# Performance work log

Hardware: AMD Instinct MI355X
Metric: run time of the kernel (lower is better)

Reference implementation:

```python
import jax, jax.numpy as jnp
import numpy as np

H = 1024          # hidden_size
I = 2048          # intermediate_size (per routed expert; shared uses I*num_shared)
E = 8             # num_routed_experts
B, S = 2, 1024


def setup_inputs() -> dict:
    key = jax.random.key(0)
    ks = jax.random.split(key, 8)
    sc_h = 1.0 / np.sqrt(H)
    sc_i = 1.0 / np.sqrt(I)
    return {
        "hidden_states": jax.random.normal(ks[0], (B, S, H), jnp.float32),
        "gate_w": jax.random.normal(ks[1], (H, E), jnp.float32) * sc_h,      # router
        "sh_gate": jax.random.normal(ks[2], (H, I), jnp.float32) * sc_h,     # shared SwiGLU
        "sh_up": jax.random.normal(ks[3], (H, I), jnp.float32) * sc_h,
        "sh_down": jax.random.normal(ks[4], (I, H), jnp.float32) * sc_i,
        "rt_gate": jax.random.normal(ks[5], (E, H, I), jnp.float32) * sc_h,  # stacked routed experts
        "rt_up": jax.random.normal(ks[6], (E, H, I), jnp.float32) * sc_h,
        "rt_down": jax.random.normal(ks[7], (E, I, H), jnp.float32) * sc_i,
    }


def _swiglu(x, wg, wu, wd):
    return (jax.nn.silu(x @ wg) * (x @ wu)) @ wd


def reference(hidden_states, gate_w, sh_gate, sh_up, sh_down, rt_gate, rt_up, rt_down):
    b, s, h = hidden_states.shape
    x = hidden_states.reshape(-1, h)                      # [T, H]
    logits = x @ gate_w                                   # [T, E]
    # top-1 routing: score = sigmoid(max logit), expert = argmax
    top_val = jnp.max(logits, axis=-1, keepdims=True)     # [T, 1]
    top_id = jnp.argmax(logits, axis=-1)                  # [T]
    score = jax.nn.sigmoid(top_val)
    xs = x * score                                        # scale tokens BEFORE expert (Llama4)
    # exact dense-masked equivalent of sort/dispatch/per-expert SwiGLU/scatter-combine:
    # every expert is applied to all tokens, then the one-hot mask selects the
    # assigned expert's output per token (identical math to ragged dispatch).
    g = jnp.einsum('th,ehi->eti', xs, rt_gate)            # [E, T, I]
    u = jnp.einsum('th,ehi->eti', xs, rt_up)
    act = jax.nn.silu(g) * u
    y = jnp.einsum('eti,eih->eth', act, rt_down)          # [E, T, H]
    onehot = jax.nn.one_hot(top_id, E, dtype=x.dtype)     # [T, E]
    routed = jnp.einsum('eth,te->th', y, onehot)          # [T, H]
    shared = _swiglu(x, sh_gate, sh_up, sh_down)          # [T, H]
    return (shared + routed).reshape(b, s, h)
```

## Files before the change

### kernel.cpp

```cpp
#include <hip/hip_runtime.h>
#include <cstdint>
#include <cstddef>

#define T_TOK 2048
#define HDIM  1024
#define IDIM  2048
#define NEXP  8

#define BM 128
#define BK1 32
#define BK2 64
#define BN2 64
#define MAXPAD 3072
#define SH_TILES 16
#define RT_TILES 24

typedef __attribute__((ext_vector_type(8))) short short8;
typedef __attribute__((ext_vector_type(4))) short short4v;
typedef __attribute__((ext_vector_type(4))) float float4v;

__device__ __forceinline__ short f2bf(float f) {
  uint32_t u = __float_as_uint(f);
  u += 0x7fffu + ((u >> 16) & 1u);
  return (short)(u >> 16);
}

__device__ __forceinline__ void gload_lds16(const void* g, void* l) {
  __builtin_amdgcn_global_load_lds(
      (const __attribute__((address_space(1))) uint32_t*)g,
      (__attribute__((address_space(3))) uint32_t*)l, 16, 0, 0);
}

__device__ __forceinline__ int swz(int c) { return c ^ ((c >> 4) & 3); }
__device__ __forceinline__ int swz64(int c) { return c ^ ((c >> 3) & 7); }


__global__ __launch_bounds__(256) void zero_init(int* __restrict__ counts,
                                                 int* __restrict__ perm) {
  int i = threadIdx.x;
  if (i < NEXP) counts[i] = 0;
  for (int p = i; p < MAXPAD; p += 256) perm[p] = 0;
}

__global__ __launch_bounds__(256) void router_kernel(
    const float* __restrict__ x, const float* __restrict__ gw,
    short* __restrict__ xbf, short* __restrict__ xsbf,
    int* __restrict__ expert_id, int* __restrict__ slot,
    int* __restrict__ counts) {
  int wv = threadIdx.x >> 6, lane = threadIdx.x & 63;
  int t = blockIdx.x * 4 + wv;
  const float* xr = x + (size_t)t * HDIM;
  float4v xv[4];
  float lg[NEXP];
#pragma unroll
  for (int e = 0; e < NEXP; e++) lg[e] = 0.f;
#pragma unroll
  for (int p = 0; p < 4; p++) {
    xv[p] = *(const float4v*)(xr + p * 256 + lane * 4);
#pragma unroll
    for (int c = 0; c < 4; c++) {
      int h = p * 256 + lane * 4 + c;
      float4v g0 = *(const float4v*)(gw + (size_t)h * NEXP);
      float4v g1 = *(const float4v*)(gw + (size_t)h * NEXP + 4);
      float xc = xv[p][c];
      lg[0] += xc * g0[0]; lg[1] += xc * g0[1];
      lg[2] += xc * g0[2]; lg[3] += xc * g0[3];
      lg[4] += xc * g1[0]; lg[5] += xc * g1[1];
      lg[6] += xc * g1[2]; lg[7] += xc * g1[3];
    }
  }
#pragma unroll
  for (int ofs = 1; ofs < 64; ofs <<= 1) {
#pragma unroll
    for (int e = 0; e < NEXP; e++) lg[e] += __shfl_xor(lg[e], ofs, 64);
  }
  int be = 0;
  float bv = lg[0];
#pragma unroll
  for (int e = 1; e < NEXP; e++) {
    if (lg[e] > bv) { bv = lg[e]; be = e; }
  }
  float score = 1.f / (1.f + __expf(-bv));
  if (lane == 0) {
    expert_id[t] = be;
    slot[t] = atomicAdd(&counts[be], 1);
  }
#pragma unroll
  for (int p = 0; p < 4; p++) {
    short4v b, bs;
#pragma unroll
    for (int c = 0; c < 4; c++) {
      b[c] = f2bf(xv[p][c]);
      bs[c] = f2bf(xv[p][c] * score);
    }
    *(short4v*)(xbf + (size_t)t * HDIM + p * 256 + lane * 4) = b;
    *(short4v*)(xsbf + (size_t)t * HDIM + p * 256 + lane * 4) = bs;
  }
}

__global__ void prefix_kernel(const int* __restrict__ counts, int* __restrict__ pad_off) {
  if (threadIdx.x == 0 && blockIdx.x == 0) {
    int run = 0;
    for (int e = 0; e < NEXP; e++) {
      pad_off[e] = run;
      run += (counts[e] + BM - 1) & ~(BM - 1);
    }
    pad_off[NEXP] = run;
  }
}

__global__ __launch_bounds__(256) void build_perm(
    const int* __restrict__ expert_id, const int* __restrict__ slot,
    const int* __restrict__ pad_off, int* __restrict__ perm) {
  int t = blockIdx.x * 256 + threadIdx.x;
  int e = expert_id[t];
  perm[pad_off[e] + slot[t]] = t;
}


__global__ __launch_bounds__(256) void transpose_all(
    const float* __restrict__ shg, const float* __restrict__ shu,
    const float* __restrict__ rtg, const float* __restrict__ rtu,
    short* __restrict__ shg_t, short* __restrict__ shu_t,
    short* __restrict__ rtg_t, short* __restrict__ rtu_t,
    const float* __restrict__ shd, const float* __restrict__ rtd,
    short* __restrict__ shd_t, short* __restrict__ rtd_t) {
  __shared__ __align__(16) short t[64][66];
  int zz = blockIdx.z;
  int tid = threadIdx.x;
  int tr = tid >> 4, tc = (tid & 15) * 4;
  int oc = tid >> 2, rs = (tid & 3) * 16;
  if (zz < 9) {
    const float *s0, *s1;
    short *d0, *d1;
    if (zz == 0) { s0 = shg; s1 = shu; d0 = shg_t; d1 = shu_t; }
    else {
      size_t o = (size_t)(zz - 1) * HDIM * IDIM;
      s0 = rtg + o; s1 = rtu + o; d0 = rtg_t + o; d1 = rtu_t + o;
    }
    const int R = HDIM, C = IDIM;
    int r0 = blockIdx.y * 64, c0 = blockIdx.x * 64;
#pragma unroll
    for (int pass = 0; pass < 2; pass++) {
      const float* s = pass ? s1 : s0;
      short* d = pass ? d1 : d0;
      if (pass) __syncthreads();
#pragma unroll
      for (int i = 0; i < 4; i++) {
        float4v v = *(const float4v*)(s + (size_t)(r0 + tr + i * 16) * C + c0 + tc);
        int w0 = (int)(unsigned short)f2bf(v[0]) | ((int)f2bf(v[1]) << 16);
        int w1 = (int)(unsigned short)f2bf(v[2]) | ((int)f2bf(v[3]) << 16);
        int* p = (int*)&t[tr + i * 16][tc];
        p[0] = w0;
        p[1] = w1;
      }
      __syncthreads();
      short8 o0, o1;
#pragma unroll
      for (int j = 0; j < 8; j++) { o0[j] = t[rs + j][oc]; o1[j] = t[rs + 8 + j][oc]; }
      short* dp = d + (size_t)(c0 + oc) * R + r0 + rs;
      *(short8*)dp = o0;
      *(short8*)(dp + 8) = o1;
    }
  } else {
    int z = zz - 9;
    const float* s = (z == 0) ? shd : rtd + (size_t)(z - 1) * IDIM * HDIM;
    short* d = (z == 0) ? shd_t : rtd_t + (size_t)(z - 1) * IDIM * HDIM;
    const int R = IDIM, C = HDIM;
    int r0 = blockIdx.x * 64, c0 = blockIdx.y * 64;
#pragma unroll
    for (int i = 0; i < 4; i++) {
      float4v v = *(const float4v*)(s + (size_t)(r0 + tr + i * 16) * C + c0 + tc);
      int w0 = (int)(unsigned short)f2bf(v[0]) | ((int)f2bf(v[1]) << 16);
      int w1 = (int)(unsigned short)f2bf(v[2]) | ((int)f2bf(v[3]) << 16);
      int* p = (int*)&t[tr + i * 16][tc];
      p[0] = w0;
      p[1] = w1;
    }
    __syncthreads();
    short8 o0, o1;
#pragma unroll
    for (int j = 0; j < 8; j++) { o0[j] = t[rs + j][oc]; o1[j] = t[rs + 8 + j][oc]; }
    short* dp = d + (size_t)(c0 + oc) * R + r0 + rs;
    *(short8*)dp = o0;
    *(short8*)(dp + 8) = o1;
  }
}


__global__ __launch_bounds__(256) void gemm1_swiglu(
    const short* __restrict__ xbf, const short* __restrict__ xsbf,
    const short* __restrict__ shg_t, const short* __restrict__ shu_t,
    const short* __restrict__ rtg_t, const short* __restrict__ rtu_t,
    short* __restrict__ act_sh, short* __restrict__ act_rt,
    const int* __restrict__ pad_off, const int* __restrict__ perm) {
  __shared__ __align__(1024) short sA[2][BM * BK1];
  __shared__ __align__(1024) short sBg[2][BM * BK1];
  __shared__ __align__(1024) short sBu[2][BM * BK1];
  int tid = threadIdx.x, lane = tid & 63, wv = tid >> 6;
  int C0 = blockIdx.x * 128;
  int y = blockIdx.y;
  const short *A, *Bg, *Bu;
  short* act;
  int R0;
  bool routed = (y >= SH_TILES);
  if (!routed) {
    A = xbf; Bg = shg_t; Bu = shu_t; act = act_sh; R0 = y * BM;
  } else {
    R0 = (y - SH_TILES) * BM;
    if (R0 >= pad_off[NEXP]) return;
    int e = 0;
    while (pad_off[e + 1] <= R0) e++;
    size_t o = (size_t)e * HDIM * IDIM;
    A = xsbf; Bg = rtg_t + o; Bu = rtu_t + o; act = act_rt;
  }
  int c0 = swz(tid), c1 = swz(tid + 256);
  int r0c = c0 >> 2, r1c = c1 >> 2;
  int ar0 = routed ? perm[R0 + r0c] : R0 + r0c;
  int ar1 = routed ? perm[R0 + r1c] : R0 + r1c;
  size_t gA0 = (size_t)ar0 * HDIM + (c0 & 3) * 8;
  size_t gA1 = (size_t)ar1 * HDIM + (c1 & 3) * 8;
  size_t gB0 = (size_t)(C0 + r0c) * HDIM + (c0 & 3) * 8;
  size_t gB1 = (size_t)(C0 + r1c) * HDIM + (c1 & 3) * 8;

  float4v accg[4][4], accu[4][4];
  float4v z4 = {0.f, 0.f, 0.f, 0.f};
#pragma unroll
  for (int i = 0; i < 4; i++)
#pragma unroll
    for (int j = 0; j < 4; j++) { accg[i][j] = z4; accu[i][j] = z4; }

  const int wrow = (wv >> 1) * 64, wcol = (wv & 1) * 64;
  const int mrow = lane & 15, h4 = lane >> 4;
  int aoff[4], boff[4];
#pragma unroll
  for (int i = 0; i < 4; i++)
    aoff[i] = swz(((wrow + i * 16 + mrow) << 2) + h4) * 8;
#pragma unroll
  for (int j = 0; j < 4; j++)
    boff[j] = swz(((wcol + j * 16 + mrow) << 2) + h4) * 8;

  gload_lds16(A + gA0, sA[0] + tid * 8);
  gload_lds16(A + gA1, sA[0] + (tid + 256) * 8);
  gload_lds16(Bg + gB0, sBg[0] + tid * 8);
  gload_lds16(Bg + gB1, sBg[0] + (tid + 256) * 8);
  gload_lds16(Bu + gB0, sBu[0] + tid * 8);
  gload_lds16(Bu + gB1, sBu[0] + (tid + 256) * 8);

  int cur = 0;
  for (int k0 = 0; k0 < HDIM; k0 += BK1) {
    __syncthreads();
    int kn = k0 + BK1;
    if (kn < HDIM) {
      short* nA = sA[cur ^ 1];
      short* nG = sBg[cur ^ 1];
      short* nU = sBu[cur ^ 1];
      gload_lds16(A + gA0 + kn, nA + tid * 8);
      gload_lds16(A + gA1 + kn, nA + (tid + 256) * 8);
      gload_lds16(Bg + gB0 + kn, nG + tid * 8);
      gload_lds16(Bg + gB1 + kn, nG + (tid + 256) * 8);
      gload_lds16(Bu + gB0 + kn, nU + tid * 8);
      gload_lds16(Bu + gB1 + kn, nU + (tid + 256) * 8);
    }
    const short* cA = sA[cur];
    const short* cG = sBg[cur];
    const short* cU = sBu[cur];
    short8 af[4], bg[4], bu[4];
#pragma unroll
    for (int i = 0; i < 4; i++) af[i] = *(const short8*)(cA + aoff[i]);
#pragma unroll
    for (int j = 0; j < 4; j++) {
      bg[j] = *(const short8*)(cG + boff[j]);
      bu[j] = *(const short8*)(cU + boff[j]);
    }
#pragma unroll
    for (int i = 0; i < 4; i++)
#pragma unroll
      for (int j = 0; j < 4; j++) {
        accg[i][j] = __builtin_amdgcn_mfma_f32_16x16x32_bf16(af[i], bg[j], accg[i][j], 0, 0, 0);
        accu[i][j] = __builtin_amdgcn_mfma_f32_16x16x32_bf16(af[i], bu[j], accu[i][j], 0, 0, 0);
      }
    cur ^= 1;
  }
  int qrow = h4 * 4, col = mrow;
#pragma unroll
  for (int i = 0; i < 4; i++)
#pragma unroll
    for (int j = 0; j < 4; j++)
#pragma unroll
      for (int r = 0; r < 4; r++) {
        int row = R0 + wrow + i * 16 + qrow + r;
        int c = C0 + wcol + j * 16 + col;
        float g = accg[i][j][r], u = accu[i][j][r];
        float sv = g / (1.f + __expf(-g)) * u;
        act[(size_t)row * IDIM + c] = f2bf(sv);
      }
}


__global__ __launch_bounds__(256) void gemm2_down(
    const short* __restrict__ act_sh, const short* __restrict__ act_rt,
    const short* __restrict__ shd_t, const short* __restrict__ rtd_t,
    float* __restrict__ out, float* __restrict__ rt_out,
    const int* __restrict__ pad_off, const int* __restrict__ counts,
    const int* __restrict__ perm) {
  __shared__ __align__(1024) short sA[2][BM * BK2];
  __shared__ __align__(1024) short sB[2][BN2 * BK2];
  int tid = threadIdx.x, lane = tid & 63, wv = tid >> 6;
  int C0 = blockIdx.x * BN2;
  int y = blockIdx.y;
  const short *A, *Bd;
  int R0, e = 0;
  bool routed = (y >= SH_TILES);
  if (!routed) {
    A = act_sh; Bd = shd_t; R0 = y * BM;
  } else {
    R0 = (y - SH_TILES) * BM;
    if (R0 >= pad_off[NEXP]) return;
    while (pad_off[e + 1] <= R0) e++;
    A = act_rt; Bd = rtd_t + (size_t)e * IDIM * HDIM;
  }
  size_t gA[4], gB[2];
#pragma unroll
  for (int q = 0; q < 4; q++) {
    int c = swz64(tid + 256 * q);
    gA[q] = (size_t)(R0 + (c >> 3)) * IDIM + (c & 7) * 8;
  }
#pragma unroll
  for (int q = 0; q < 2; q++) {
    int c = swz64(tid + 256 * q);
    gB[q] = (size_t)(C0 + (c >> 3)) * IDIM + (c & 7) * 8;
  }

  float4v acc[2][4];
  float4v z4 = {0.f, 0.f, 0.f, 0.f};
#pragma unroll
  for (int i = 0; i < 2; i++)
#pragma unroll
    for (int j = 0; j < 4; j++) acc[i][j] = z4;

  const int wrow = wv * 32;
  const int mrow = lane & 15, h4 = lane >> 4;
  int aoff[2][2], boff[4][2];
#pragma unroll
  for (int i = 0; i < 2; i++)
#pragma unroll
    for (int ks = 0; ks < 2; ks++)
      aoff[i][ks] = swz64(((wrow + i * 16 + mrow) << 3) + ks * 4 + h4) * 8;
#pragma unroll
  for (int j = 0; j < 4; j++)
#pragma unroll
    for (int ks = 0; ks < 2; ks++)
      boff[j][ks] = swz64(((j * 16 + mrow) << 3) + ks * 4 + h4) * 8;

#pragma unroll
  for (int q = 0; q < 4; q++) gload_lds16(A + gA[q], sA[0] + (tid + 256 * q) * 8);
#pragma unroll
  for (int q = 0; q < 2; q++) gload_lds16(Bd + gB[q], sB[0] + (tid + 256 * q) * 8);

  int cur = 0;
  for (int k0 = 0; k0 < IDIM; k0 += BK2) {
    __syncthreads();
    int kn = k0 + BK2;
    if (kn < IDIM) {
      short* nA = sA[cur ^ 1];
      short* nB = sB[cur ^ 1];
#pragma unroll
      for (int q = 0; q < 4; q++) gload_lds16(A + gA[q] + kn, nA + (tid + 256 * q) * 8);
#pragma unroll
      for (int q = 0; q < 2; q++) gload_lds16(Bd + gB[q] + kn, nB + (tid + 256 * q) * 8);
    }
    const short* cA = sA[cur];
    const short* cB = sB[cur];
#pragma unroll
    for (int ks = 0; ks < 2; ks++) {
      short8 af[2], bf4[4];
#pragma unroll
      for (int i = 0; i < 2; i++) af[i] = *(const short8*)(cA + aoff[i][ks]);
#pragma unroll
      for (int j = 0; j < 4; j++) bf4[j] = *(const short8*)(cB + boff[j][ks]);
#pragma unroll
      for (int i = 0; i < 2; i++)
#pragma unroll
        for (int j = 0; j < 4; j++)
          acc[i][j] = __builtin_amdgcn_mfma_f32_16x16x32_bf16(af[i], bf4[j], acc[i][j], 0, 0, 0);
    }
    cur ^= 1;
  }
  int qrow = h4 * 4, col = mrow;
#pragma unroll
  for (int i = 0; i < 2; i++)
#pragma unroll
    for (int j = 0; j < 4; j++)
#pragma unroll
      for (int r = 0; r < 4; r++) {
        int row = R0 + wrow + i * 16 + qrow + r;
        int c = C0 + j * 16 + col;
        float v = acc[i][j][r];
        if (!routed) {
          out[(size_t)row * HDIM + c] = v;
        } else if (row - pad_off[e] < counts[e]) {
          rt_out[(size_t)perm[row] * HDIM + c] = v;
        }
      }
}

__global__ __launch_bounds__(256) void add_routed(float* __restrict__ out,
                                                  const float* __restrict__ rt_out) {
  size_t i = ((size_t)blockIdx.x * 256 + threadIdx.x) * 4;
  float4v a = *(const float4v*)(out + i);
  float4v b = *(const float4v*)(rt_out + i);
  a[0] += b[0]; a[1] += b[1]; a[2] += b[2]; a[3] += b[3];
  *(float4v*)(out + i) = a;
}


extern "C" void kernel_launch(void* const* d_in, const int* in_sizes, int n_in,
                              void* d_out, int out_size, void* d_ws, size_t ws_size,
                              hipStream_t stream) {
  const float* x       = (const float*)d_in[0];
  const float* gate_w  = (const float*)d_in[1];
  const float* sh_gate = (const float*)d_in[2];
  const float* sh_up   = (const float*)d_in[3];
  const float* sh_down = (const float*)d_in[4];
  const float* rt_gate = (const float*)d_in[5];
  const float* rt_up   = (const float*)d_in[6];
  const float* rt_down = (const float*)d_in[7];
  float* out = (float*)d_out;

  char* w = (char*)d_ws;
  const size_t MB = 1024 * 1024;
  short* xbf    = (short*)(w + 0 * MB);
  short* xsbf   = (short*)(w + 4 * MB);
  short* act_sh = (short*)(w + 8 * MB);
  short* act_rt = (short*)(w + 16 * MB);
  float* rt_out = (float*)(w + 28 * MB);
  short* shg_t  = (short*)(w + 36 * MB);
  short* shu_t  = (short*)(w + 40 * MB);
  short* shd_t  = (short*)(w + 44 * MB);
  short* rtg_t  = (short*)(w + 48 * MB);
  short* rtu_t  = (short*)(w + 80 * MB);
  short* rtd_t  = (short*)(w + 112 * MB);
  int* ints     = (int*)(w + 144 * MB);
  int* counts    = ints;
  int* pad_off   = ints + 8;
  int* expert_id = ints + 32;
  int* slot      = ints + 32 + 2048;
  int* perm      = ints + 32 + 4096;

  zero_init<<<1, 256, 0, stream>>>(counts, perm);
  router_kernel<<<T_TOK / 4, 256, 0, stream>>>(x, gate_w, xbf, xsbf, expert_id, slot, counts);
  prefix_kernel<<<1, 64, 0, stream>>>(counts, pad_off);
  build_perm<<<T_TOK / 256, 256, 0, stream>>>(expert_id, slot, pad_off, perm);

  transpose_all<<<dim3(32, 16, 18), 256, 0, stream>>>(
      sh_gate, sh_up, rt_gate, rt_up, shg_t, shu_t, rtg_t, rtu_t,
      sh_down, rt_down, shd_t, rtd_t);

  gemm1_swiglu<<<dim3(IDIM / 128, SH_TILES + RT_TILES), 256, 0, stream>>>(
      xbf, xsbf, shg_t, shu_t, rtg_t, rtu_t, act_sh, act_rt, pad_off, perm);

  gemm2_down<<<dim3(HDIM / BN2, SH_TILES + RT_TILES), 256, 0, stream>>>(
      act_sh, act_rt, shd_t, rtd_t, out, rt_out, pad_off, counts, perm);

  add_routed<<<(T_TOK * HDIM) / (256 * 4), 256, 0, stream>>>(out, rt_out);
}
```

Before: 424.1 us.

## Triple-buffer both GEMMs with explicit vmcnt waits and 512-thread gemm1

Both GEMM kernels move from double-buffered LDS staging with __syncthreads to a three-stage ring. Explicit s_waitcnt vmcnt and raw s_barrier let two tiles of loads stay in flight while MFMAs run, and s_setprio raises wave priority around the MFMA block. gemm1 now uses 512 threads with 8 waves, each computing a 64x32 subtile, and gemm2's K step drops from 64 to 32 to fit the extra buffer. This is meant to hide global-load latency and raise occupancy, at the cost of more barriers per unit of K work and halved per-wave reuse in gemm1.

```diff
diff --git a/kernel.cpp b/kernel.cpp
--- a/kernel.cpp
+++ b/kernel.cpp
@@ -9,7 +9,7 @@
 
 #define BM 128
 #define BK1 32
-#define BK2 64
+#define BK2 32
 #define BN2 64
 #define MAXPAD 3072
 #define SH_TILES 16
@@ -32,7 +32,6 @@
 }
 
 __device__ __forceinline__ int swz(int c) { return c ^ ((c >> 4) & 3); }
-__device__ __forceinline__ int swz64(int c) { return c ^ ((c >> 3) & 7); }
 
 
 __global__ __launch_bounds__(256) void zero_init(int* __restrict__ counts,
@@ -188,15 +187,20 @@
 }
 
 
-__global__ __launch_bounds__(256) void gemm1_swiglu(
+#define G1_STAGE(b, kk) do { \
+    gload_lds16(A + gA + (kk), sA[b] + tid * 8);   \
+    gload_lds16(Bg + gB + (kk), sBg[b] + tid * 8); \
+    gload_lds16(Bu + gB + (kk), sBu[b] + tid * 8); } while (0)
+
+__global__ __launch_bounds__(512, 2) void gemm1_swiglu(
     const short* __restrict__ xbf, const short* __restrict__ xsbf,
     const short* __restrict__ shg_t, const short* __restrict__ shu_t,
     const short* __restrict__ rtg_t, const short* __restrict__ rtu_t,
     short* __restrict__ act_sh, short* __restrict__ act_rt,
     const int* __restrict__ pad_off, const int* __restrict__ perm) {
-  __shared__ __align__(1024) short sA[2][BM * BK1];
-  __shared__ __align__(1024) short sBg[2][BM * BK1];
-  __shared__ __align__(1024) short sBu[2][BM * BK1];
+  __shared__ __align__(1024) short sA[3][BM * BK1];
+  __shared__ __align__(1024) short sBg[3][BM * BK1];
+  __shared__ __align__(1024) short sBu[3][BM * BK1];
   int tid = threadIdx.x, lane = tid & 63, wv = tid >> 6;
   int C0 = blockIdx.x * 128;
   int y = blockIdx.y;
@@ -214,79 +218,72 @@
     size_t o = (size_t)e * HDIM * IDIM;
     A = xsbf; Bg = rtg_t + o; Bu = rtu_t + o; act = act_rt;
   }
-  int c0 = swz(tid), c1 = swz(tid + 256);
-  int r0c = c0 >> 2, r1c = c1 >> 2;
+  int c0 = swz(tid);
+  int r0c = c0 >> 2;
   int ar0 = routed ? perm[R0 + r0c] : R0 + r0c;
-  int ar1 = routed ? perm[R0 + r1c] : R0 + r1c;
-  size_t gA0 = (size_t)ar0 * HDIM + (c0 & 3) * 8;
-  size_t gA1 = (size_t)ar1 * HDIM + (c1 & 3) * 8;
-  size_t gB0 = (size_t)(C0 + r0c) * HDIM + (c0 & 3) * 8;
-  size_t gB1 = (size_t)(C0 + r1c) * HDIM + (c1 & 3) * 8;
-
-  float4v accg[4][4], accu[4][4];
+  size_t gA = (size_t)ar0 * HDIM + (c0 & 3) * 8;
+  size_t gB = (size_t)(C0 + r0c) * HDIM + (c0 & 3) * 8;
+
+  float4v accg[4][2], accu[4][2];
   float4v z4 = {0.f, 0.f, 0.f, 0.f};
 #pragma unroll
   for (int i = 0; i < 4; i++)
 #pragma unroll
-    for (int j = 0; j < 4; j++) { accg[i][j] = z4; accu[i][j] = z4; }
-
-  const int wrow = (wv >> 1) * 64, wcol = (wv & 1) * 64;
+    for (int j = 0; j < 2; j++) { accg[i][j] = z4; accu[i][j] = z4; }
+
+  const int wrow = (wv >> 2) * 64, wcol = (wv & 3) * 32;
   const int mrow = lane & 15, h4 = lane >> 4;
-  int aoff[4], boff[4];
+  int aoff[4], boff[2];
 #pragma unroll
   for (int i = 0; i < 4; i++)
     aoff[i] = swz(((wrow + i * 16 + mrow) << 2) + h4) * 8;
 #pragma unroll
-  for (int j = 0; j < 4; j++)
+  for (int j = 0; j < 2; j++)
     boff[j] = swz(((wcol + j * 16 + mrow) << 2) + h4) * 8;
 
-  gload_lds16(A + gA0, sA[0] + tid * 8);
-  gload_lds16(A + gA1, sA[0] + (tid + 256) * 8);
-  gload_lds16(Bg + gB0, sBg[0] + tid * 8);
-  gload_lds16(Bg + gB1, sBg[0] + (tid + 256) * 8);
-  gload_lds16(Bu + gB0, sBu[0] + tid * 8);
-  gload_lds16(Bu + gB1, sBu[0] + (tid + 256) * 8);
+  G1_STAGE(0, 0);
+  G1_STAGE(1, BK1);
 
   int cur = 0;
   for (int k0 = 0; k0 < HDIM; k0 += BK1) {
-    __syncthreads();
-    int kn = k0 + BK1;
-    if (kn < HDIM) {
-      short* nA = sA[cur ^ 1];
-      short* nG = sBg[cur ^ 1];
-      short* nU = sBu[cur ^ 1];
-      gload_lds16(A + gA0 + kn, nA + tid * 8);
-      gload_lds16(A + gA1 + kn, nA + (tid + 256) * 8);
-      gload_lds16(Bg + gB0 + kn, nG + tid * 8);
-      gload_lds16(Bg + gB1 + kn, nG + (tid + 256) * 8);
-      gload_lds16(Bu + gB0 + kn, nU + tid * 8);
-      gload_lds16(Bu + gB1 + kn, nU + (tid + 256) * 8);
+    if (k0 + BK1 < HDIM) {
+      asm volatile("s_waitcnt vmcnt(3)" ::: "memory");
+    } else {
+      asm volatile("s_waitcnt vmcnt(0)" ::: "memory");
+    }
+    __builtin_amdgcn_s_barrier();
+    int k2 = k0 + 2 * BK1;
+    if (k2 < HDIM) {
+      int nb = cur + 2; if (nb >= 3) nb -= 3;
+      G1_STAGE(nb, k2);
     }
     const short* cA = sA[cur];
     const short* cG = sBg[cur];
     const short* cU = sBu[cur];
-    short8 af[4], bg[4], bu[4];
+    short8 af[4], bg[2], bu[2];
 #pragma unroll
     for (int i = 0; i < 4; i++) af[i] = *(const short8*)(cA + aoff[i]);
 #pragma unroll
-    for (int j = 0; j < 4; j++) {
+    for (int j = 0; j < 2; j++) {
       bg[j] = *(const short8*)(cG + boff[j]);
       bu[j] = *(const short8*)(cU + boff[j]);
     }
+    __builtin_amdgcn_s_setprio(1);
 #pragma unroll
     for (int i = 0; i < 4; i++)
 #pragma unroll
-      for (int j = 0; j < 4; j++) {
+      for (int j = 0; j < 2; j++) {
         accg[i][j] = __builtin_amdgcn_mfma_f32_16x16x32_bf16(af[i], bg[j], accg[i][j], 0, 0, 0);
         accu[i][j] = __builtin_amdgcn_mfma_f32_16x16x32_bf16(af[i], bu[j], accu[i][j], 0, 0, 0);
       }
-    cur ^= 1;
+    __builtin_amdgcn_s_setprio(0);
+    cur = (cur == 2) ? 0 : cur + 1;
   }
   int qrow = h4 * 4, col = mrow;
 #pragma unroll
   for (int i = 0; i < 4; i++)
 #pragma unroll
-    for (int j = 0; j < 4; j++)
+    for (int j = 0; j < 2; j++)
 #pragma unroll
       for (int r = 0; r < 4; r++) {
         int row = R0 + wrow + i * 16 + qrow + r;
@@ -298,14 +295,19 @@
 }
 
 
-__global__ __launch_bounds__(256) void gemm2_down(
+#define G2_STAGE(b, kk) do { \
+    gload_lds16(A + gA0 + (kk), sA[b] + tid * 8);         \
+    gload_lds16(A + gA1 + (kk), sA[b] + (tid + 256) * 8); \
+    gload_lds16(Bd + gB0 + (kk), sB[b] + tid * 8); } while (0)
+
+__global__ __launch_bounds__(256, 4) void gemm2_down(
     const short* __restrict__ act_sh, const short* __restrict__ act_rt,
     const short* __restrict__ shd_t, const short* __restrict__ rtd_t,
     float* __restrict__ out, float* __restrict__ rt_out,
     const int* __restrict__ pad_off, const int* __restrict__ counts,
     const int* __restrict__ perm) {
-  __shared__ __align__(1024) short sA[2][BM * BK2];
-  __shared__ __align__(1024) short sB[2][BN2 * BK2];
+  __shared__ __align__(1024) short sA[3][BM * BK2];
+  __shared__ __align__(1024) short sB[3][BN2 * BK2];
   int tid = threadIdx.x, lane = tid & 63, wv = tid >> 6;
   int C0 = blockIdx.x * BN2;
   int y = blockIdx.y;
@@ -320,17 +322,10 @@
     while (pad_off[e + 1] <= R0) e++;
     A = act_rt; Bd = rtd_t + (size_t)e * IDIM * HDIM;
   }
-  size_t gA[4], gB[2];
-#pragma unroll
-  for (int q = 0; q < 4; q++) {
-    int c = swz64(tid + 256 * q);
-    gA[q] = (size_t)(R0 + (c >> 3)) * IDIM + (c & 7) * 8;
-  }
-#pragma unroll
-  for (int q = 0; q < 2; q++) {
-    int c = swz64(tid + 256 * q);
-    gB[q] = (size_t)(C0 + (c >> 3)) * IDIM + (c & 7) * 8;
-  }
+  int cA0 = swz(tid), cA1 = swz(tid + 256), cB = swz(tid);
+  size_t gA0 = (size_t)(R0 + (cA0 >> 2)) * IDIM + (cA0 & 3) * 8;
+  size_t gA1 = (size_t)(R0 + (cA1 >> 2)) * IDIM + (cA1 & 3) * 8;
+  size_t gB0 = (size_t)(C0 + (cB >> 2)) * IDIM + (cB & 3) * 8;
 
   float4v acc[2][4];
   float4v z4 = {0.f, 0.f, 0.f, 0.f};
@@ -341,51 +336,45 @@
 
   const int wrow = wv * 32;
   const int mrow = lane & 15, h4 = lane >> 4;
-  int aoff[2][2], boff[4][2];
+  int aoff[2], boff[4];
 #pragma unroll
   for (int i = 0; i < 2; i++)
-#pragma unroll
-    for (int ks = 0; ks < 2; ks++)
-      aoff[i][ks] = swz64(((wrow + i * 16 + mrow) << 3) + ks * 4 + h4) * 8;
+    aoff[i] = swz(((wrow + i * 16 + mrow) << 2) + h4) * 8;
 #pragma unroll
   for (int j = 0; j < 4; j++)
-#pragma unroll
-    for (int ks = 0; ks < 2; ks++)
-      boff[j][ks] = swz64(((j * 16 + mrow) << 3) + ks * 4 + h4) * 8;
-
-#pragma unroll
-  for (int q = 0; q < 4; q++) gload_lds16(A + gA[q], sA[0] + (tid + 256 * q) * 8);
-#pragma unroll
-  for (int q = 0; q < 2; q++) gload_lds16(Bd + gB[q], sB[0] + (tid + 256 * q) * 8);
+    boff[j] = swz(((j * 16 + mrow) << 2) + h4) * 8;
+
+  G2_STAGE(0, 0);
+  G2_STAGE(1, BK2);
 
   int cur = 0;
   for (int k0 = 0; k0 < IDIM; k0 += BK2) {
-    __syncthreads();
-    int kn = k0 + BK2;
-    if (kn < IDIM) {
-      short* nA = sA[cur ^ 1];
-      short* nB = sB[cur ^ 1];
-#pragma unroll
-      for (int q = 0; q < 4; q++) gload_lds16(A + gA[q] + kn, nA + (tid + 256 * q) * 8);
-#pragma unroll
-      for (int q = 0; q < 2; q++) gload_lds16(Bd + gB[q] + kn, nB + (tid + 256 * q) * 8);
-    }
-    const short* cA = sA[cur];
-    const short* cB = sB[cur];
-#pragma unroll
-    for (int ks = 0; ks < 2; ks++) {
-      short8 af[2], bf4[4];
-#pragma unroll
-      for (int i = 0; i < 2; i++) af[i] = *(const short8*)(cA + aoff[i][ks]);
-#pragma unroll
-      for (int j = 0; j < 4; j++) bf4[j] = *(const short8*)(cB + boff[j][ks]);
-#pragma unroll
-      for (int i = 0; i < 2; i++)
-#pragma unroll
-        for (int j = 0; j < 4; j++)
-          acc[i][j] = __builtin_amdgcn_mfma_f32_16x16x32_bf16(af[i], bf4[j], acc[i][j], 0, 0, 0);
-    }
-    cur ^= 1;
+    if (k0 + BK2 < IDIM) {
+      asm volatile("s_waitcnt vmcnt(3)" ::: "memory");
+    } else {
+      asm volatile("s_waitcnt vmcnt(0)" ::: "memory");
+    }
+    __builtin_amdgcn_s_barrier();
+    int k2 = k0 + 2 * BK2;
+    if (k2 < IDIM) {
+      int nb = cur + 2; if (nb >= 3) nb -= 3;
+      G2_STAGE(nb, k2);
+    }
+    const short* cAp = sA[cur];
+    const short* cBp = sB[cur];
+    short8 af[2], bf4[4];
+#pragma unroll
+    for (int i = 0; i < 2; i++) af[i] = *(const short8*)(cAp + aoff[i]);
+#pragma unroll
+    for (int j = 0; j < 4; j++) bf4[j] = *(const short8*)(cBp + boff[j]);
+    __builtin_amdgcn_s_setprio(1);
+#pragma unroll
+    for (int i = 0; i < 2; i++)
+#pragma unroll
+      for (int j = 0; j < 4; j++)
+        acc[i][j] = __builtin_amdgcn_mfma_f32_16x16x32_bf16(af[i], bf4[j], acc[i][j], 0, 0, 0);
+    __builtin_amdgcn_s_setprio(0);
+    cur = (cur == 2) ? 0 : cur + 1;
   }
   int qrow = h4 * 4, col = mrow;
 #pragma unroll
@@ -457,7 +446,7 @@
       sh_gate, sh_up, rt_gate, rt_up, shg_t, shu_t, rtg_t, rtu_t,
       sh_down, rt_down, shd_t, rtd_t);
 
-  gemm1_swiglu<<<dim3(IDIM / 128, SH_TILES + RT_TILES), 256, 0, stream>>>(
+  gemm1_swiglu<<<dim3(IDIM / 128, SH_TILES + RT_TILES), 512, 0, stream>>>(
       xbf, xsbf, shg_t, shu_t, rtg_t, rtu_t, act_sh, act_rt, pad_off, perm);
 
   gemm2_down<<<dim3(HDIM / BN2, SH_TILES + RT_TILES), 256, 0, stream>>>(
```

Measured after the change: 401.2 us. 1.06x faster.
